# Kernel optimization log

Measured on AMD Instinct MI355X. Metric: run time of the kernel, lower is better.

## Reference

```python
import jax, jax.numpy as jnp
import numpy as np

N = 1024  # num boxes (labels == predictions count so diff == 0 branch)


def jaccard(box_a, box_b):
    # box_a: [A,4], box_b: [B,4], xyxy format -> IoU matrix [A,B]
    max_xy = jnp.minimum(box_a[:, None, 2:], box_b[None, :, 2:])
    min_xy = jnp.maximum(box_a[:, None, :2], box_b[None, :, :2])
    inter_wh = jnp.clip(max_xy - min_xy, 0.0)
    inter = inter_wh[..., 0] * inter_wh[..., 1]
    area_a = ((box_a[:, 2] - box_a[:, 0]) * (box_a[:, 3] - box_a[:, 1]))[:, None]
    area_b = ((box_b[:, 2] - box_b[:, 0]) * (box_b[:, 3] - box_b[:, 1]))[None, :]
    return inter / (area_a + area_b - inter)


def greedy_match(JM):
    """Replicates the original greedy loop: N steps; each step takes the LAST
    row-major-order maximal entry ('>=' update) among rows/cols not in `seen`,
    swaps label rows r<->c (tracked via perm), and marks column c as seen."""
    n = JM.shape[0]
    MASKED = jnp.float32(-1.0)  # IoU >= 0, so -1 excludes masked entries

    def body(carry, _):
        perm, seen = carry
        M = JM[perm]                                  # rows permuted with labels
        mask = seen[:, None] | seen[None, :]          # one `seen` set for rows & cols
        vals = jnp.where(mask, MASKED, M).reshape(-1)
        # last occurrence of the max (the '>=' in the Python loop keeps the latest)
        i = vals.shape[0] - 1 - jnp.argmax(vals[::-1])
        r, c = i // n, i % n
        pr, pc = perm[r], perm[c]
        perm = perm.at[r].set(pc).at[c].set(pr)
        seen = seen.at[c].set(True)
        return (perm, seen), None

    init = (jnp.arange(n), jnp.zeros(n, dtype=bool))
    (perm, _), _ = jax.lax.scan(body, init, None, length=n)
    return perm


def setup_inputs() -> dict:
    key = jax.random.key(0)
    k1, k2, k3, k4, k5 = jax.random.split(key, 5)
    # valid xyxy boxes: x2 > x1, y2 > y1
    lmin = jax.random.uniform(k1, (N, 2), dtype=jnp.float32)
    lwh = jax.random.uniform(k2, (N, 2), dtype=jnp.float32) * 0.2 + 0.01
    labels = jnp.concatenate([lmin, lmin + lwh], axis=-1)
    pmin = jax.random.uniform(k3, (N, 2), dtype=jnp.float32)
    pwh = jax.random.uniform(k4, (N, 2), dtype=jnp.float32) * 0.2 + 0.01
    predictions = jnp.concatenate([pmin, pmin + pwh], axis=-1)
    scores = jax.random.normal(k5, (N,), dtype=jnp.float32)
    return {"predictions": predictions, "labels": labels, "scores": scores}


def reference(predictions, labels, scores):
    # L == P -> diff == 0, no truncation, scores untouched.
    JM = jaccard(labels, predictions)
    perm = greedy_match(JM)
    labels_matched = labels[perm]
    # F.l1_loss default reduction: mean over all elements.
    # NOTE: the original's `loss.add(F.cross_entropy(...))` is non-in-place and
    # its result is discarded, so the CE term does NOT contribute; diff == 0 so
    # the diff*4 branch is skipped. Faithfully: loss = L1 only.
    loss = jnp.mean(jnp.abs(labels_matched - predictions))
    return loss
```

## Files before the change

### kernel.cpp

```cpp
#include <hip/hip_runtime.h>
#include <stdint.h>

#define NBOX 1024
#define UNK  0xFFFFFFFFFFFFFFFFull

typedef unsigned long long u64;
typedef unsigned int u32;
typedef unsigned short u16;
typedef unsigned char u8;

__device__ __forceinline__ float iou_pair(const float4 lb, float larea,
                                          const float4 pb, float parea) {
    float ix1 = fmaxf(lb.x, pb.x);
    float iy1 = fmaxf(lb.y, pb.y);
    float ix2 = fminf(lb.z, pb.z);
    float iy2 = fminf(lb.w, pb.w);
    float w = fmaxf(__fsub_rn(ix2, ix1), 0.0f);
    float h = fmaxf(__fsub_rn(iy2, iy1), 0.0f);
    float inter = __fmul_rn(w, h);
    float denom = __fsub_rn(__fadd_rn(larea, parea), inter);
    return inter / denom;
}

__device__ __forceinline__ u64 umax64(u64 a, u64 b) { return a > b ? a : b; }
__device__ __forceinline__ u64 umin64(u64 a, u64 b) { return a < b ? a : b; }

__device__ __forceinline__ u64 dpp_max64(u64 v) {
    unsigned lo, hi; u64 o;
#define DPP_STEP(CTRL) \
    lo = (unsigned)__builtin_amdgcn_update_dpp(0, (int)(unsigned)(v & 0xffffffffull), CTRL, 0xf, 0xf, true); \
    hi = (unsigned)__builtin_amdgcn_update_dpp(0, (int)(unsigned)(v >> 32),           CTRL, 0xf, 0xf, true); \
    o = (((u64)hi) << 32) | lo; \
    if (o > v) v = o;
    DPP_STEP(0x111) DPP_STEP(0x112) DPP_STEP(0x114)
    DPP_STEP(0x118) DPP_STEP(0x142) DPP_STEP(0x143)
#undef DPP_STEP
    return v;
}

__device__ __forceinline__ void dpp_top2(u64 &a1, u64 &a2) {
    unsigned lo, hi; u64 b1, b2, min1;
#define T2STEP(CTRL) \
    lo = (unsigned)__builtin_amdgcn_update_dpp(0, (int)(unsigned)(a1 & 0xffffffffull), CTRL, 0xf, 0xf, true); \
    hi = (unsigned)__builtin_amdgcn_update_dpp(0, (int)(unsigned)(a1 >> 32),           CTRL, 0xf, 0xf, true); \
    b1 = (((u64)hi) << 32) | lo; \
    lo = (unsigned)__builtin_amdgcn_update_dpp(0, (int)(unsigned)(a2 & 0xffffffffull), CTRL, 0xf, 0xf, true); \
    hi = (unsigned)__builtin_amdgcn_update_dpp(0, (int)(unsigned)(a2 >> 32),           CTRL, 0xf, 0xf, true); \
    b2 = (((u64)hi) << 32) | lo; \
    min1 = (b1 == a1) ? 0ull : umin64(a1, b1); \
    a1 = umax64(a1, b1); \
    a2 = umax64(umax64(a2, b2), min1);
    T2STEP(0x111) T2STEP(0x112) T2STEP(0x114) T2STEP(0x118) T2STEP(0x142) T2STEP(0x143)
#undef T2STEP
}

__device__ __forceinline__ u64 readlane64(u64 v, int l) {
    unsigned lo = (unsigned)__builtin_amdgcn_readlane((int)(unsigned)(v & 0xffffffffull), l);
    unsigned hi = (unsigned)__builtin_amdgcn_readlane((int)(unsigned)(v >> 32), l);
    return (((u64)hi) << 32) | lo;
}

__global__ void __launch_bounds__(64) jm_init(const float* __restrict__ labels,
                                              const float* __restrict__ preds,
                                              float* __restrict__ JM,
                                              u64* __restrict__ rkey_ws,
                                              u64* __restrict__ rkey2_ws) {
    const int b = blockIdx.x;
    const int lane = threadIdx.x;
    float4 lb = ((const float4*)labels)[b];
    float la = __fmul_rn(__fsub_rn(lb.z, lb.x), __fsub_rn(lb.w, lb.y));
    u64 a1 = 0, a2 = 0;
    #pragma unroll
    for (int m = 0; m < 4; ++m) {
        float4 v;
        float* vv = (float*)&v;
        #pragma unroll
        for (int k = 0; k < 4; ++k) {
            int c = 4 * lane + 256 * m + k;
            float4 pb = ((const float4*)preds)[c];
            float pa = __fmul_rn(__fsub_rn(pb.z, pb.x), __fsub_rn(pb.w, pb.y));
            vv[k] = iou_pair(lb, la, pb, pa);
        }
        if (JM) ((float4*)JM)[b * 256 + lane + 64 * m] = v;
        #pragma unroll
        for (int k = 0; k < 4; ++k) {
            int c = 4 * lane + 256 * m + k;
            u64 p = ((u64)__float_as_uint(vv[k]) << 10) | (unsigned)c;
            a2 = umax64(a2, umin64(a1, p));
            a1 = umax64(a1, p);
        }
    }
    dpp_top2(a1, a2);
    if (lane == 63) {
        if ((a1 >> 10) == 0ull) { rkey_ws[b] = 0ull; rkey2_ws[b] = 0ull; }
        else { rkey_ws[b] = a1; rkey2_ws[b] = (a2 >> 10) ? a2 : 0ull; }
    }
}

__global__ void __launch_bounds__(64) init_colmax(const float* __restrict__ labels,
                                                  const float* __restrict__ preds,
                                                  float* __restrict__ JMT,
                                                  u64* __restrict__ cub_ws) {
    const int c = blockIdx.x;
    const int lane = threadIdx.x;
    float4 pc = ((const float4*)preds)[c];
    float pa = __fmul_rn(__fsub_rn(pc.z, pc.x), __fsub_rn(pc.w, pc.y));
    u64 best = 0; u32 v1 = 0, v2 = 0;
    #pragma unroll
    for (int j = 0; j < 16; ++j) {
        int L = lane + (j << 6);
        float4 lb = ((const float4*)labels)[L];
        float la = __fmul_rn(__fsub_rn(lb.z, lb.x), __fsub_rn(lb.w, lb.y));
        float v = iou_pair(lb, la, pc, pa);
        if (JMT) JMT[(size_t)c * NBOX + L] = v;
        u32 vb = __float_as_uint(v);
        if (vb >= v1) { v2 = v1; v1 = vb; } else { v2 = (vb > v2) ? vb : v2; }
        best = umax64(best, ((u64)vb << 10) | (unsigned)L);
    }
    best = dpp_max64(best);
    u64 bm = readlane64(best, 63);
    u32 V = (u32)(bm >> 10);
    u64 b1 = __ballot(v1 == V);
    u64 b2 = __ballot(v2 == V);
    bool tie = (__popcll(b1) >= 2) || (b2 != 0ull);
    if (lane == 63)
        cub_ws[c] = V ? (((u64)V << 32) | (tie ? (1ull << 16) : 0ull) | (bm & 1023ull))
                      : 0ull;
}

__global__ void __launch_bounds__(1024, 1)
rounds_kernel(const float* __restrict__ preds,
              const float* __restrict__ labels,
              const float* __restrict__ JM,
              const float* __restrict__ JMT,
              const u64* __restrict__ rkey_ws,
              const u64* __restrict__ rkey2_ws,
              const u64* __restrict__ cub_ws,
              float* __restrict__ out) {
    __shared__ float4 pred4s[NBOX];
    __shared__ float4 lab4s[NBOX];
    __shared__ float  parea_s[NBOX];
    __shared__ float  larea_s[NBOX];
    __shared__ u64    rkey[NBOX];
    __shared__ u64    rkey2[NBOX];
    __shared__ u64    cub[NBOX];
    __shared__ u64    colbest[NBOX];
    __shared__ u16    pos_s[NBOX];
    __shared__ u16    dest_s[NBOX];
    __shared__ u16    perm_s[NBOX];
    __shared__ u8     seenc[NBOX];
    __shared__ u8     lockedl[NBOX];
    __shared__ u32    seenw[32];
    __shared__ u32    lockedw[32];
    __shared__ int    ncommit;
    __shared__ float  fpart[16];

    const int t    = (int)threadIdx.x;
    const int lane = t & 63;
    const int wid  = t >> 6;

    {
        float4 p = ((const float4*)preds)[t];
        float4 L = ((const float4*)labels)[t];
        pred4s[t] = p;
        lab4s[t]  = L;
        parea_s[t] = __fmul_rn(__fsub_rn(p.z, p.x), __fsub_rn(p.w, p.y));
        larea_s[t] = __fmul_rn(__fsub_rn(L.z, L.x), __fsub_rn(L.w, L.y));
        pos_s[t] = (u16)t; perm_s[t] = (u16)t; dest_s[t] = 0;
        seenc[t] = 0; lockedl[t] = 0;
        rkey[t]  = rkey_ws  ? rkey_ws[t]  : 0ull;
        rkey2[t] = rkey2_ws ? rkey2_ws[t] : UNK;
        cub[t]   = cub_ws   ? cub_ws[t]   : 0ull;
        colbest[t] = 0ull;
        if (t < 32) { seenw[t] = 0u; lockedw[t] = 0u; }
        if (t == 0) ncommit = 0;
    }
    __syncthreads();

    u32 myseen = 0;
    u32 mylocked = 0;

    auto scan_row = [&](int L, u64 &r1, u64 &r2) {
        u64 a1 = 0, a2 = 0;
        if (JM) {
            const float4* row4 = (const float4*)(JM + (size_t)L * NBOX);
            #pragma unroll
            for (int m = 0; m < 4; ++m) {
                float4 f = row4[lane + 64 * m];
                float* ff = (float*)&f;
                #pragma unroll
                for (int k = 0; k < 4; ++k) {
                    int cc = 4 * lane + 256 * m + k;
                    u64 p = ((u64)__float_as_uint(ff[k]) << 10) | (unsigned)cc;
                    if ((myseen >> ((m << 2) | k)) & 1u) p = 0;
                    a2 = umax64(a2, umin64(a1, p));
                    a1 = umax64(a1, p);
                }
            }
        } else {
            float4 lb = lab4s[L];
            float la = larea_s[L];
            #pragma unroll
            for (int m = 0; m < 4; ++m) {
                #pragma unroll
                for (int k = 0; k < 4; ++k) {
                    int cc = 4 * lane + 256 * m + k;
                    float v = iou_pair(lb, la, pred4s[cc], parea_s[cc]);
                    u64 p = ((u64)__float_as_uint(v) << 10) | (unsigned)cc;
                    if ((myseen >> ((m << 2) | k)) & 1u) p = 0;
                    a2 = umax64(a2, umin64(a1, p));
                    a1 = umax64(a1, p);
                }
            }
        }
        dpp_top2(a1, a2);
        r1 = a1; r2 = a2;
    };

    auto scan_col = [&](int c) -> u64 {
        u64 best = 0; u32 v1 = 0, v2 = 0;
        if (JMT) {
            const float4* col4 = (const float4*)(JMT + (size_t)c * NBOX);
            #pragma unroll
            for (int m = 0; m < 4; ++m) {
                float4 f = col4[lane + 64 * m];
                float* ff = (float*)&f;
                #pragma unroll
                for (int k = 0; k < 4; ++k) {
                    int L = 4 * lane + 256 * m + k;
                    u32 vb = __float_as_uint(ff[k]);
                    if ((mylocked >> ((m << 2) | k)) & 1u) vb = 0;
                    if (vb >= v1) { v2 = v1; v1 = vb; } else { v2 = (vb > v2) ? vb : v2; }
                    u64 key = ((u64)vb << 20) | ((u64)pos_s[L] << 10) | (unsigned)L;
                    if (!vb) key = 0;
                    best = umax64(best, key);
                }
            }
        } else {
            float4 pc = pred4s[c];
            float  pa = parea_s[c];
            #pragma unroll
            for (int m = 0; m < 4; ++m) {
                #pragma unroll
                for (int k = 0; k < 4; ++k) {
                    int L = 4 * lane + 256 * m + k;
                    float v = iou_pair(lab4s[L], larea_s[L], pc, pa);
                    u32 vb = __float_as_uint(v);
                    if ((mylocked >> ((m << 2) | k)) & 1u) vb = 0;
                    if (vb >= v1) { v2 = v1; v1 = vb; } else { v2 = (vb > v2) ? vb : v2; }
                    u64 key = ((u64)vb << 20) | ((u64)pos_s[L] << 10) | (unsigned)L;
                    if (!vb) key = 0;
                    best = umax64(best, key);
                }
            }
        }
        best = dpp_max64(best);
        u64 bm = readlane64(best, 63);
        u32 V = (u32)(bm >> 20);
        u64 b1 = __ballot(v1 == V);
        u64 b2 = __ballot(v2 == V);
        bool tie = (__popcll(b1) >= 2) || (b2 != 0ull);
        return V ? (((u64)V << 32) | (tie ? (1ull << 16) : 0ull) | (bm & 1023ull)) : 0ull;
    };

    if (!rkey_ws) {
        for (int L = wid; L < NBOX; L += 16) {
            u64 r1, r2; scan_row(L, r1, r2);
            if (lane == 63) {
                if ((r1 >> 10) == 0ull) { rkey[L] = 0ull; rkey2[L] = 0ull; }
                else { rkey[L] = r1; rkey2[L] = (r2 >> 10) ? r2 : 0ull; }
            }
        }
        for (int c = wid; c < NBOX; c += 16) {
            u64 cbv = scan_col(c);
            if (lane == 0) cub[c] = cbv;
        }
        __syncthreads();
    }

    for (int round = 0; round < 2048; ++round) {
        {
            u64 k = rkey[t];
            if (k) atomicMax((unsigned long long*)&colbest[k & 1023ull],
                             ((k >> 10) << 20) | ((u64)pos_s[t] << 10) | (u64)(unsigned)t);
            if (t == 0) ncommit = 0;
        }
        __syncthreads();

        {
            bool need = false;
            u64 sb = colbest[t];
            if (sb) {
                u32 sval = (u32)(sb >> 20);
                u32 slab = (u32)(sb & 1023ull);
                u64 cb = cub[t];
                u32 cval = (u32)(cb >> 32);
                u32 clab = (u32)(cb & 1023ull);
                bool ctie = (cb >> 16) & 1ull;
                if (lockedl[clab] || ctie || (sval == cval && slab != clab)) {
                    need = true;
                } else if (slab == clab) {
                    int c = t, L = (int)slab;
                    seenc[c] = 1; lockedl[L] = 1; rkey[L] = 0ull;
                    dest_s[L] = (u16)c; perm_s[c] = (u16)L;
                    atomicOr(&seenw[c >> 5], 1u << (c & 31));
                    atomicOr(&lockedw[L >> 5], 1u << (L & 31));
                    atomicAdd(&ncommit, 1);
                }
            }
            u64 bal = __ballot(need);
            while (bal) {
                int l = (int)__ffsll(bal) - 1;
                bal &= bal - 1;
                int c = (wid << 6) | l;
                u64 cbv = scan_col(c);
                if (lane == 0) {
                    cub[c] = cbv;
                    u64 sb2 = colbest[c];
                    if (sb2 && cbv && (u32)(cbv & 1023ull) == (u32)(sb2 & 1023ull)) {
                        int L = (int)(sb2 & 1023ull);
                        seenc[c] = 1; lockedl[L] = 1; rkey[L] = 0ull;
                        dest_s[L] = (u16)c; perm_s[c] = (u16)L;
                        atomicOr(&seenw[c >> 5], 1u << (c & 31));
                        atomicOr(&lockedw[L >> 5], 1u << (L & 31));
                        atomicAdd(&ncommit, 1);
                    }
                }
            }
        }
        __syncthreads();

        const int nc = ncommit;
        {
            u32 ms = 0, ml = 0;
            #pragma unroll
            for (int m = 0; m < 4; ++m) {
                u32 ws_ = seenw[(lane >> 3) + (m << 3)];
                u32 wl  = lockedw[(lane >> 3) + (m << 3)];
                u32 sh  = (lane & 7) << 2;
                ms |= ((ws_ >> sh) & 0xFu) << (m << 2);
                ml |= ((wl  >> sh) & 0xFu) << (m << 2);
            }
            myseen = ms; mylocked = ml;
        }
        {
            bool needrow = false;
            u64 k = rkey[t];
            if (k && seenc[k & 1023ull]) {
                u64 k2 = rkey2[t];
                if (k2 != UNK) {
                    rkey[t] = k2;
                    rkey2[t] = UNK;
                    if (k2 && seenc[k2 & 1023ull]) needrow = true;
                } else {
                    needrow = true;
                }
            }
            u64 bal = __ballot(needrow);
            while (bal) {
                int l = (int)__ffsll(bal) - 1;
                bal &= bal - 1;
                int row = (wid << 6) | l;
                u64 r1, r2; scan_row(row, r1, r2);
                if (lane == 63) {
                    if ((r1 >> 10) == 0ull) { rkey[row] = 0ull; rkey2[row] = 0ull; }
                    else { rkey[row] = r1; rkey2[row] = (r2 >> 10) ? r2 : 0ull; }
                }
            }
        }
        colbest[t] = 0ull;
        if (!seenc[t]) {
            int l = (int)perm_s[t];
            while (lockedl[l]) l = (int)dest_s[l];
            pos_s[l] = (u16)t;
            perm_s[t] = (u16)l;
        }
        __syncthreads();

        if (nc == 0) break;
    }

    {
        float4 lb = lab4s[perm_s[t]];
        float4 pb = pred4s[t];
        float sum = fabsf(lb.x - pb.x) + fabsf(lb.y - pb.y) +
                    fabsf(lb.z - pb.z) + fabsf(lb.w - pb.w);
        for (int off = 32; off > 0; off >>= 1) sum += __shfl_xor(sum, off, 64);
        if (lane == 0) fpart[wid] = sum;
        __syncthreads();
        if (t == 0) {
            float s = 0.0f;
            for (int w = 0; w < 16; ++w) s += fpart[w];
            out[0] = s * (1.0f / 4096.0f);
        }
    }
}

extern "C" void kernel_launch(void* const* d_in, const int* in_sizes, int n_in,
                              void* d_out, int out_size, void* d_ws, size_t ws_size,
                              hipStream_t stream) {
    const float* preds  = (const float*)d_in[0];
    const float* labels = (const float*)d_in[1];
    float* out = (float*)d_out;

    const size_t jm_b   = (size_t)NBOX * NBOX * sizeof(float);
    const size_t keys_b = 3 * NBOX * sizeof(u64);

    float *JM = nullptr, *JMT = nullptr;
    u64 *rk = nullptr, *rk2 = nullptr, *cb = nullptr;
    char* w = (char*)d_ws;

    if (d_ws && ws_size >= 2 * jm_b + keys_b) {
        JM  = (float*)w;
        JMT = (float*)(w + jm_b);
        rk  = (u64*)(w + 2 * jm_b); rk2 = rk + NBOX; cb = rk2 + NBOX;
    } else if (d_ws && ws_size >= jm_b + keys_b) {
        JM  = (float*)w;
        rk  = (u64*)(w + jm_b); rk2 = rk + NBOX; cb = rk2 + NBOX;
    } else if (d_ws && ws_size >= keys_b) {
        rk  = (u64*)w; rk2 = rk + NBOX; cb = rk2 + NBOX;
    }

    if (rk) {
        jm_init<<<NBOX, 64, 0, stream>>>(labels, preds, JM, rk, rk2);
        init_colmax<<<NBOX, 64, 0, stream>>>(labels, preds, JMT, cb);
    }
    rounds_kernel<<<1, 1024, 0, stream>>>(preds, labels, JM, JMT, rk, rk2, cb, out);
}
```

Measured before the change: 246.0 us.

## Process row and column rescans in pairs with 32-bit top-2 reductions

Row and column rescans now handle two rows or columns per wavefront pass, which interleaves two independent loads and reductions to hide latency. Per-lane top-2 tracking moves from packed 64-bit keys to 32-bit value/index pairs. Cross-row reductions use DPP row shifts plus four readlanes in place of the full DPP chain. Column scans take a cheaper value-only path and fall back to the exact tie-aware scan only when the top two values tie. This adds register pressure and code complexity, and it could change tie-break semantics if the fast path differs from the exact ordering.

Measured after the change: 229.5 us. 6.7% less time.

```diff
diff --git a/kernel.cpp b/kernel.cpp
--- a/kernel.cpp
+++ b/kernel.cpp
@@ -59,6 +59,29 @@
     unsigned hi = (unsigned)__builtin_amdgcn_readlane((int)(unsigned)(v >> 32), l);
     return (((u64)hi) << 32) | lo;
 }
+__device__ __forceinline__ u32 readlane32(u32 v, int l) {
+    return (u32)__builtin_amdgcn_readlane((int)v, l);
+}
+
+#define SHR_T2_STEP(a1, a2, CTRL) { \
+    unsigned _lo, _hi; u64 _b1, _b2, _mn; \
+    _lo = (unsigned)__builtin_amdgcn_update_dpp(0, (int)(unsigned)((a1) & 0xffffffffull), CTRL, 0xf, 0xf, true); \
+    _hi = (unsigned)__builtin_amdgcn_update_dpp(0, (int)(unsigned)((a1) >> 32),           CTRL, 0xf, 0xf, true); \
+    _b1 = (((u64)_hi) << 32) | _lo; \
+    _lo = (unsigned)__builtin_amdgcn_update_dpp(0, (int)(unsigned)((a2) & 0xffffffffull), CTRL, 0xf, 0xf, true); \
+    _hi = (unsigned)__builtin_amdgcn_update_dpp(0, (int)(unsigned)((a2) >> 32),           CTRL, 0xf, 0xf, true); \
+    _b2 = (((u64)_hi) << 32) | _lo; \
+    _mn = umin64((a1), _b1); \
+    (a1) = umax64((a1), _b1); \
+    (a2) = umax64(umax64((a2), _b2), _mn); }
+
+#define SHR_V2_STEP(v1, v2, CTRL) { \
+    u32 _s1 = (u32)__builtin_amdgcn_update_dpp(0, (int)(v1), CTRL, 0xf, 0xf, true); \
+    u32 _s2 = (u32)__builtin_amdgcn_update_dpp(0, (int)(v2), CTRL, 0xf, 0xf, true); \
+    u32 _mn = (v1) < _s1 ? (v1) : _s1; \
+    (v1) = (v1) > _s1 ? (v1) : _s1; \
+    u32 _m2 = (v2) > _s2 ? (v2) : _s2; \
+    (v2) = _m2 > _mn ? _m2 : _mn; }
 
 __global__ void __launch_bounds__(64) jm_init(const float* __restrict__ labels,
                                               const float* __restrict__ preds,
@@ -180,51 +203,100 @@
     u32 myseen = 0;
     u32 mylocked = 0;
 
-    auto scan_row = [&](int L, u64 &r1, u64 &r2) {
-        u64 a1 = 0, a2 = 0;
+    auto scan_row2 = [&](int La, int Lb, bool hb,
+                         u64 &r1a, u64 &r2a, u64 &r1b, u64 &r2b) {
+        u32 av1 = 0, ac1 = 0, av2 = 0, ac2 = 0;
+        u32 bv1 = 0, bc1 = 0, bv2 = 0, bc2 = 0;
         if (JM) {
-            const float4* row4 = (const float4*)(JM + (size_t)L * NBOX);
+            const float4* A4 = (const float4*)(JM + (size_t)La * NBOX);
+            const float4* B4 = (const float4*)(JM + (size_t)Lb * NBOX);
             #pragma unroll
             for (int m = 0; m < 4; ++m) {
-                float4 f = row4[lane + 64 * m];
-                float* ff = (float*)&f;
+                float4 fa = A4[lane + 64 * m];
+                float4 fb = B4[lane + 64 * m];
+                const float* qa = (const float*)&fa;
+                const float* qb = (const float*)&fb;
                 #pragma unroll
                 for (int k = 0; k < 4; ++k) {
-                    int cc = 4 * lane + 256 * m + k;
-                    u64 p = ((u64)__float_as_uint(ff[k]) << 10) | (unsigned)cc;
-                    if ((myseen >> ((m << 2) | k)) & 1u) p = 0;
-                    a2 = umax64(a2, umin64(a1, p));
-                    a1 = umax64(a1, p);
+                    u32 cc = (u32)(4 * lane + 256 * m + k);
+                    bool msk = (myseen >> ((m << 2) | k)) & 1u;
+                    u32 va = __float_as_uint(qa[k]);
+                    u32 vb = __float_as_uint(qb[k]);
+                    if (!msk && va) {
+                        if (va >= av1) { av2 = av1; ac2 = ac1; av1 = va; ac1 = cc; }
+                        else if (va >= av2) { av2 = va; ac2 = cc; }
+                    }
+                    if (!msk && vb) {
+                        if (vb >= bv1) { bv2 = bv1; bc2 = bc1; bv1 = vb; bc1 = cc; }
+                        else if (vb >= bv2) { bv2 = vb; bc2 = cc; }
+                    }
                 }
             }
         } else {
-            float4 lb = lab4s[L];
-            float la = larea_s[L];
+            float4 lba = lab4s[La]; float laa = larea_s[La];
+            float4 lbb = lab4s[Lb]; float lbb_a = larea_s[Lb];
             #pragma unroll
             for (int m = 0; m < 4; ++m) {
                 #pragma unroll
                 for (int k = 0; k < 4; ++k) {
-                    int cc = 4 * lane + 256 * m + k;
-                    float v = iou_pair(lb, la, pred4s[cc], parea_s[cc]);
-                    u64 p = ((u64)__float_as_uint(v) << 10) | (unsigned)cc;
-                    if ((myseen >> ((m << 2) | k)) & 1u) p = 0;
-                    a2 = umax64(a2, umin64(a1, p));
-                    a1 = umax64(a1, p);
-                }
-            }
-        }
-        dpp_top2(a1, a2);
-        r1 = a1; r2 = a2;
+                    u32 cc = (u32)(4 * lane + 256 * m + k);
+                    bool msk = (myseen >> ((m << 2) | k)) & 1u;
+                    u32 va = __float_as_uint(iou_pair(lba, laa, pred4s[cc], parea_s[cc]));
+                    u32 vb = __float_as_uint(iou_pair(lbb, lbb_a, pred4s[cc], parea_s[cc]));
+                    if (!msk && va) {
+                        if (va >= av1) { av2 = av1; ac2 = ac1; av1 = va; ac1 = cc; }
+                        else if (va >= av2) { av2 = va; ac2 = cc; }
+                    }
+                    if (!msk && vb) {
+                        if (vb >= bv1) { bv2 = bv1; bc2 = bc1; bv1 = vb; bc1 = cc; }
+                        else if (vb >= bv2) { bv2 = vb; bc2 = cc; }
+                    }
+                }
+            }
+        }
+        u64 a1 = ((u64)av1 << 10) | ac1, a2 = ((u64)av2 << 10) | ac2;
+        u64 b1 = ((u64)bv1 << 10) | bc1, b2 = ((u64)bv2 << 10) | bc2;
+        SHR_T2_STEP(a1, a2, 0x111) SHR_T2_STEP(b1, b2, 0x111)
+        SHR_T2_STEP(a1, a2, 0x112) SHR_T2_STEP(b1, b2, 0x112)
+        SHR_T2_STEP(a1, a2, 0x114) SHR_T2_STEP(b1, b2, 0x114)
+        SHR_T2_STEP(a1, a2, 0x118) SHR_T2_STEP(b1, b2, 0x118)
+        {
+            u64 p1 = readlane64(a1, 15), p2 = readlane64(a2, 15);
+            u64 q1 = readlane64(a1, 31), q2 = readlane64(a2, 31);
+            u64 s1 = readlane64(a1, 47), s2 = readlane64(a2, 47);
+            u64 w1 = readlane64(a1, 63), w2 = readlane64(a2, 63);
+            u64 mn = umin64(p1, q1); p1 = umax64(p1, q1); p2 = umax64(umax64(p2, q2), mn);
+            mn = umin64(s1, w1); s1 = umax64(s1, w1); s2 = umax64(umax64(s2, w2), mn);
+            mn = umin64(p1, s1); p1 = umax64(p1, s1); p2 = umax64(umax64(p2, s2), mn);
+            r1a = p1; r2a = p2;
+        }
+        if (hb) {
+            u64 p1 = readlane64(b1, 15), p2 = readlane64(b2, 15);
+            u64 q1 = readlane64(b1, 31), q2 = readlane64(b2, 31);
+            u64 s1 = readlane64(b1, 47), s2 = readlane64(b2, 47);
+            u64 w1 = readlane64(b1, 63), w2 = readlane64(b2, 63);
+            u64 mn = umin64(p1, q1); p1 = umax64(p1, q1); p2 = umax64(umax64(p2, q2), mn);
+            mn = umin64(s1, w1); s1 = umax64(s1, w1); s2 = umax64(umax64(s2, w2), mn);
+            mn = umin64(p1, s1); p1 = umax64(p1, s1); p2 = umax64(umax64(p2, s2), mn);
+            r1b = p1; r2b = p2;
+        } else { r1b = 0; r2b = 0; }
     };
 
-    auto scan_col = [&](int c) -> u64 {
+    auto store_rkey = [&](int L, u64 r1, u64 r2) {
+        if (lane == 0) {
+            if ((r1 >> 10) == 0ull) { rkey[L] = 0ull; rkey2[L] = 0ull; }
+            else { rkey[L] = r1; rkey2[L] = (r2 >> 10) ? r2 : 0ull; }
+        }
+    };
+
+    auto scan_col_exact = [&](int c) -> u64 {
         u64 best = 0; u32 v1 = 0, v2 = 0;
         if (JMT) {
             const float4* col4 = (const float4*)(JMT + (size_t)c * NBOX);
             #pragma unroll
             for (int m = 0; m < 4; ++m) {
                 float4 f = col4[lane + 64 * m];
-                float* ff = (float*)&f;
+                const float* ff = (const float*)&f;
                 #pragma unroll
                 for (int k = 0; k < 4; ++k) {
                     int L = 4 * lane + 256 * m + k;
@@ -263,17 +335,126 @@
         return V ? (((u64)V << 32) | (tie ? (1ull << 16) : 0ull) | (bm & 1023ull)) : 0ull;
     };
 
+    auto scan_col2 = [&](int ca, int cb, bool hb, u64 &oa, u64 &ob) {
+        u32 av1 = 0, av2 = 0, al1 = 0;
+        u32 bv1 = 0, bv2 = 0, bl1 = 0;
+        if (JMT) {
+            const float4* A4 = (const float4*)(JMT + (size_t)ca * NBOX);
+            const float4* B4 = (const float4*)(JMT + (size_t)cb * NBOX);
+            #pragma unroll
+            for (int m = 0; m < 4; ++m) {
+                float4 fa = A4[lane + 64 * m];
+                float4 fb = B4[lane + 64 * m];
+                const float* qa = (const float*)&fa;
+                const float* qb = (const float*)&fb;
+                #pragma unroll
+                for (int k = 0; k < 4; ++k) {
+                    u32 L = (u32)(4 * lane + 256 * m + k);
+                    bool msk = (mylocked >> ((m << 2) | k)) & 1u;
+                    u32 va = msk ? 0u : __float_as_uint(qa[k]);
+                    u32 vb = msk ? 0u : __float_as_uint(qb[k]);
+                    if (va > av1) { av2 = av1; av1 = va; al1 = L; }
+                    else av2 = (va > av2) ? va : av2;
+                    if (vb > bv1) { bv2 = bv1; bv1 = vb; bl1 = L; }
+                    else bv2 = (vb > bv2) ? vb : bv2;
+                }
+            }
+        } else {
+            float4 pca = pred4s[ca]; float paa = parea_s[ca];
+            float4 pcb = pred4s[cb]; float pab = parea_s[cb];
+            #pragma unroll
+            for (int m = 0; m < 4; ++m) {
+                #pragma unroll
+                for (int k = 0; k < 4; ++k) {
+                    u32 L = (u32)(4 * lane + 256 * m + k);
+                    bool msk = (mylocked >> ((m << 2) | k)) & 1u;
+                    u32 va = msk ? 0u : __float_as_uint(iou_pair(lab4s[L], larea_s[L], pca, paa));
+                    u32 vb = msk ? 0u : __float_as_uint(iou_pair(lab4s[L], larea_s[L], pcb, pab));
+                    if (va > av1) { av2 = av1; av1 = va; al1 = L; }
+                    else av2 = (va > av2) ? va : av2;
+                    if (vb > bv1) { bv2 = bv1; bv1 = vb; bl1 = L; }
+                    else bv2 = (vb > bv2) ? vb : bv2;
+                }
+            }
+        }
+        u32 sva = av1, sla = al1;
+        u32 svb = bv1, slb = bl1;
+        SHR_V2_STEP(av1, av2, 0x111) SHR_V2_STEP(bv1, bv2, 0x111)
+        SHR_V2_STEP(av1, av2, 0x112) SHR_V2_STEP(bv1, bv2, 0x112)
+        SHR_V2_STEP(av1, av2, 0x114) SHR_V2_STEP(bv1, bv2, 0x114)
+        SHR_V2_STEP(av1, av2, 0x118) SHR_V2_STEP(bv1, bv2, 0x118)
+        u32 Va, V2a, Vb, V2b;
+        {
+            u32 p1 = readlane32(av1, 15), p2 = readlane32(av2, 15);
+            u32 q1 = readlane32(av1, 31), q2 = readlane32(av2, 31);
+            u32 s1 = readlane32(av1, 47), s2 = readlane32(av2, 47);
+            u32 w1 = readlane32(av1, 63), w2 = readlane32(av2, 63);
+            u32 mn = p1 < q1 ? p1 : q1; p1 = p1 > q1 ? p1 : q1;
+            p2 = p2 > q2 ? p2 : q2; p2 = p2 > mn ? p2 : mn;
+            mn = s1 < w1 ? s1 : w1; s1 = s1 > w1 ? s1 : w1;
+            s2 = s2 > w2 ? s2 : w2; s2 = s2 > mn ? s2 : mn;
+            mn = p1 < s1 ? p1 : s1; p1 = p1 > s1 ? p1 : s1;
+            p2 = p2 > s2 ? p2 : s2; p2 = p2 > mn ? p2 : mn;
+            Va = p1; V2a = p2;
+        }
+        {
+            u32 p1 = readlane32(bv1, 15), p2 = readlane32(bv2, 15);
+            u32 q1 = readlane32(bv1, 31), q2 = readlane32(bv2, 31);
+            u32 s1 = readlane32(bv1, 47), s2 = readlane32(bv2, 47);
+            u32 w1 = readlane32(bv1, 63), w2 = readlane32(bv2, 63);
+            u32 mn = p1 < q1 ? p1 : q1; p1 = p1 > q1 ? p1 : q1;
+            p2 = p2 > q2 ? p2 : q2; p2 = p2 > mn ? p2 : mn;
+            mn = s1 < w1 ? s1 : w1; s1 = s1 > w1 ? s1 : w1;
+            s2 = s2 > w2 ? s2 : w2; s2 = s2 > mn ? s2 : mn;
+            mn = p1 < s1 ? p1 : s1; p1 = p1 > s1 ? p1 : s1;
+            p2 = p2 > s2 ? p2 : s2; p2 = p2 > mn ? p2 : mn;
+            Vb = p1; V2b = p2;
+        }
+        if (Va == 0) oa = 0ull;
+        else if (V2a == Va) oa = UNK;
+        else {
+            u64 ball = __ballot(sva == Va);
+            int wl = (int)__ffsll(ball) - 1;
+            u32 lbl = readlane32(sla, wl);
+            oa = ((u64)Va << 32) | lbl;
+        }
+        if (!hb) { ob = 0ull; return; }
+        if (Vb == 0) ob = 0ull;
+        else if (V2b == Vb) ob = UNK;
+        else {
+            u64 ball = __ballot(svb == Vb);
+            int wl = (int)__ffsll(ball) - 1;
+            u32 lbl = readlane32(slb, wl);
+            ob = ((u64)Vb << 32) | lbl;
+        }
+    };
+
+    auto try_commit = [&](int c, u64 cbv) {
+        u64 sb = colbest[c];
+        if (sb && cbv && !((cbv >> 16) & 1ull) &&
+            (u32)(cbv & 1023ull) == (u32)(sb & 1023ull)) {
+            int L = (int)(sb & 1023ull);
+            seenc[c] = 1; lockedl[L] = 1; rkey[L] = 0ull;
+            dest_s[L] = (u16)c; perm_s[c] = (u16)L;
+            atomicOr(&seenw[c >> 5], 1u << (c & 31));
+            atomicOr(&lockedw[L >> 5], 1u << (L & 31));
+            atomicAdd(&ncommit, 1);
+        }
+    };
+
     if (!rkey_ws) {
-        for (int L = wid; L < NBOX; L += 16) {
-            u64 r1, r2; scan_row(L, r1, r2);
-            if (lane == 63) {
-                if ((r1 >> 10) == 0ull) { rkey[L] = 0ull; rkey2[L] = 0ull; }
-                else { rkey[L] = r1; rkey2[L] = (r2 >> 10) ? r2 : 0ull; }
-            }
-        }
-        for (int c = wid; c < NBOX; c += 16) {
-            u64 cbv = scan_col(c);
-            if (lane == 0) cub[c] = cbv;
+        for (int L = 2 * wid; L < NBOX; L += 32) {
+            u64 r1a, r2a, r1b, r2b;
+            scan_row2(L, L + 1, true, r1a, r2a, r1b, r2b);
+            store_rkey(L, r1a, r2a);
+            store_rkey(L + 1, r1b, r2b);
+        }
+        for (int c = 2 * wid; c < NBOX; c += 32) {
+            u64 oa, ob;
+            scan_col2(c, c + 1, true, oa, ob);
+            if (oa == UNK) oa = scan_col_exact(c);
+            if (ob == UNK) ob = scan_col_exact(c + 1);
+            if (lane == 0) { cub[c] = oa; cub[c + 1] = ob; }
         }
         __syncthreads();
     }
@@ -310,21 +491,17 @@
             }
             u64 bal = __ballot(need);
             while (bal) {
-                int l = (int)__ffsll(bal) - 1;
-                bal &= bal - 1;
-                int c = (wid << 6) | l;
-                u64 cbv = scan_col(c);
+                int l0 = (int)__ffsll(bal) - 1; bal &= bal - 1;
+                int l1 = l0; bool hb = false;
+                if (bal) { l1 = (int)__ffsll(bal) - 1; bal &= bal - 1; hb = true; }
+                int c0 = (wid << 6) | l0, c1 = (wid << 6) | l1;
+                u64 o0, o1;
+                scan_col2(c0, c1, hb, o0, o1);
+                if (o0 == UNK) o0 = scan_col_exact(c0);
+                if (hb && o1 == UNK) o1 = scan_col_exact(c1);
                 if (lane == 0) {
-                    cub[c] = cbv;
-                    u64 sb2 = colbest[c];
-                    if (sb2 && cbv && (u32)(cbv & 1023ull) == (u32)(sb2 & 1023ull)) {
-                        int L = (int)(sb2 & 1023ull);
-                        seenc[c] = 1; lockedl[L] = 1; rkey[L] = 0ull;
-                        dest_s[L] = (u16)c; perm_s[c] = (u16)L;
-                        atomicOr(&seenw[c >> 5], 1u << (c & 31));
-                        atomicOr(&lockedw[L >> 5], 1u << (L & 31));
-                        atomicAdd(&ncommit, 1);
-                    }
+                    cub[c0] = o0; try_commit(c0, o0);
+                    if (hb) { cub[c1] = o1; try_commit(c1, o1); }
                 }
             }
         }
@@ -358,14 +535,14 @@
             }
             u64 bal = __ballot(needrow);
             while (bal) {
-                int l = (int)__ffsll(bal) - 1;
-                bal &= bal - 1;
-                int row = (wid << 6) | l;
-                u64 r1, r2; scan_row(row, r1, r2);
-                if (lane == 63) {
-                    if ((r1 >> 10) == 0ull) { rkey[row] = 0ull; rkey2[row] = 0ull; }
-                    else { rkey[row] = r1; rkey2[row] = (r2 >> 10) ? r2 : 0ull; }
-                }
+                int l0 = (int)__ffsll(bal) - 1; bal &= bal - 1;
+                int l1 = l0; bool hb = false;
+                if (bal) { l1 = (int)__ffsll(bal) - 1; bal &= bal - 1; hb = true; }
+                int r0 = (wid << 6) | l0, r1_ = (wid << 6) | l1;
+                u64 r1a, r2a, r1b, r2b;
+                scan_row2(r0, r1_, hb, r1a, r2a, r1b, r2b);
+                store_rkey(r0, r1a, r2a);
+                if (hb) store_rkey(r1_, r1b, r2b);
             }
         }
         colbest[t] = 0ull;
```
